# Kernel optimization log

Measured on AMD Instinct MI355X. Metric: run time of the kernel, lower is better.

Reference implementation:

```python
import jax, jax.numpy as jnp
import numpy as np

B = 256      # batch
C = 512      # num_classes (independent heads)
F = 768      # BERT pooler_output dim (hard-coded in module)
D = 512      # dense_layer_size


def setup_inputs() -> dict:
    key = jax.random.key(0)
    ks = jax.random.split(key, 7)
    s1 = 1.0 / np.sqrt(F)
    s2 = 1.0 / np.sqrt(D)
    return {
        "x":  jax.random.normal(ks[0], (B, F), dtype=jnp.float32),
        "W1": jax.random.normal(ks[1], (C, F, D), dtype=jnp.float32) * s1,
        "b1": jax.random.normal(ks[2], (C, D), dtype=jnp.float32) * s1,
        "W2": jax.random.normal(ks[3], (C, D, D), dtype=jnp.float32) * s2,
        "b2": jax.random.normal(ks[4], (C, D), dtype=jnp.float32) * s2,
        "W3": jax.random.normal(ks[5], (C, D, 2), dtype=jnp.float32) * s2,
        "b3": jax.random.normal(ks[6], (C, 2), dtype=jnp.float32) * s2,
    }


def reference(x, W1, b1, W2, b2, W3, b3):
    # Batched version of the per-class Python loop:
    # each head: Linear(F,D)-ReLU-(Dropout=identity in eval)-Linear(D,D)-ReLU-Linear(D,2)
    h = jax.nn.relu(jnp.einsum('bf,cfd->bcd', x, W1) + b1[None])        # [B, C, D]
    h = jax.nn.relu(jnp.einsum('bcd,cde->bce', h, W2) + b2[None])        # [B, C, D]
    out = jnp.einsum('bcd,cde->bce', h, W3) + b3[None]                   # [B, C, 2]
    return out
```

## Files before the change

### kernel.cpp

```cpp
#include <hip/hip_runtime.h>
#include <stdint.h>

typedef float f32x4 __attribute__((ext_vector_type(4)));
typedef float f32x2 __attribute__((ext_vector_type(2)));
typedef short bf16x8 __attribute__((ext_vector_type(8)));

__device__ __forceinline__ uint32_t bf16_rne(float f) {
  uint32_t x = __float_as_uint(f);
  return (x + 0x7FFFu + ((x >> 16) & 1u)) >> 16;
}

__device__ __forceinline__ void load_lds_16B(void* lds_dst, const void* gsrc) {
  __builtin_amdgcn_global_load_lds(
      (const __attribute__((address_space(1))) unsigned int*)gsrc,
      (__attribute__((address_space(3))) unsigned int*)lds_dst, 16, 0, 0);
}

__global__ void cast_x_kernel(const float* __restrict__ x,
                              uint32_t* __restrict__ xb, int n2) {
  int i = blockIdx.x * 256 + threadIdx.x;
  if (i >= n2) return;
  f32x2 v = *(const f32x2*)(x + 2 * i);
  xb[i] = bf16_rne(v[0]) | (bf16_rne(v[1]) << 16);
}

template <int K>
__global__ __launch_bounds__(512, 2) void gemm_relu(
    const uint16_t* __restrict__ Abase, long long aClassStride,
    const float* __restrict__ Wbase, const float* __restrict__ biasBase,
    uint16_t* __restrict__ Hout) {
  constexpr int NT = K / 64;
  __shared__ uint8_t smem[2 * 49152 + 512];

  const int tid = threadIdx.x;
  const int bid = blockIdx.x;
  const int logical = ((bid & 7) << 8) | (bid >> 3);
  const int c = logical >> 2;
  const int n0 = (logical & 3) * 128;

  const uint16_t* Ab = Abase + (size_t)c * (size_t)aClassStride;
  const float* Wc = Wbase + (size_t)c * K * 512 + n0;
  const float* bcp = biasBase + (size_t)c * 512 + n0;
  uint16_t* Oc = Hout + (size_t)c * (256 * 512) + n0;

  const int l = tid & 63, w = tid >> 6;
  const int lr = l & 15, lg = l >> 4;
  const int wm = w >> 1, wn = w & 1;

  const int aoff_row = (wm * 64 + lr) * 128;
  const int boff_row = 32768 + (wn * 64 + lr) * 128;
  const int kx0 = (lg * 16) ^ ((lr & 7) << 4);

  const int bcg = tid & 31;
  const int brp = tid >> 5;

  f32x4 acc[4][4];
#pragma unroll
  for (int i = 0; i < 4; i++)
#pragma unroll
    for (int j = 0; j < 4; j++) acc[i][j] = {0.f, 0.f, 0.f, 0.f};

  auto stageA = [&](int ts, int buf) {
    uint8_t* base = smem + buf * 49152;
    const uint16_t* As = Ab + ts * 64;
#pragma unroll
    for (int i = 0; i < 4; i++) {
      int idx = tid + i * 512;
      int m = idx >> 3, cc = idx & 7;
      int ccs = cc ^ (m & 7);
      load_lds_16B(base + ((w * 64 + i * 512) << 4),
                   As + (size_t)m * K + ccs * 8);
    }
  };
  auto loadB = [&](int ts, f32x4* br) {
    const float* Ws = Wc + (size_t)(ts * 64) * 512;
    br[0] = *(const f32x4*)(Ws + (size_t)(2 * brp) * 512 + 4 * bcg);
    br[1] = *(const f32x4*)(Ws + (size_t)(2 * brp + 1) * 512 + 4 * bcg);
    br[2] = *(const f32x4*)(Ws + (size_t)(2 * brp + 32) * 512 + 4 * bcg);
    br[3] = *(const f32x4*)(Ws + (size_t)(2 * brp + 33) * 512 + 4 * bcg);
  };
  auto writeB = [&](const f32x4* br, int buf) {
    uint8_t* base = smem + buf * 49152 + 32768;
#pragma unroll
    for (int u = 0; u < 2; u++) {
      int rp = brp + u * 16;
#pragma unroll
      for (int j = 0; j < 4; j++) {
        int n = 4 * bcg + j;
        uint32_t p = bf16_rne(br[2 * u][j]) | (bf16_rne(br[2 * u + 1][j]) << 16);
        *(uint32_t*)(base + n * 128 + ((4 * rp) ^ ((n & 7) << 4))) = p;
      }
    }
  };
  auto comp = [&](int buf) {
    const uint8_t* s = smem + buf * 49152;
#pragma unroll
    for (int kk = 0; kk < 2; ++kk) {
      const int kx = kx0 ^ (kk << 6);
      bf16x8 a[4], b[4];
#pragma unroll
      for (int mf = 0; mf < 4; mf++)
        a[mf] = *(const bf16x8*)(s + aoff_row + mf * 2048 + kx);
#pragma unroll
      for (int nf = 0; nf < 4; nf++)
        b[nf] = *(const bf16x8*)(s + boff_row + nf * 2048 + kx);
#pragma unroll
      for (int mf = 0; mf < 4; mf++)
#pragma unroll
        for (int nf = 0; nf < 4; nf++)
          acc[mf][nf] = __builtin_amdgcn_mfma_f32_16x16x32_bf16(
              a[mf], b[nf], acc[mf][nf], 0, 0, 0);
    }
  };

  f32x4 brA[4], brB[4];
  stageA(0, 0);
  loadB(0, brA);
  if (tid < 128) ((float*)(smem + 98304))[tid] = bcp[tid];
  writeB(brA, 0);
  __syncthreads();
  stageA(1, 1);
  loadB(1, brB);

#pragma unroll 1
  for (int t = 0; t < NT; t += 2) {
    comp(0);
    writeB(brB, 1);
    __syncthreads();
    if (t + 2 < NT) { stageA(t + 2, 0); loadB(t + 2, brA); }
    comp(1);
    if (t + 2 < NT) {
      writeB(brA, 0);
      __syncthreads();
      if (t + 3 < NT) { stageA(t + 3, 1); loadB(t + 3, brB); }
    }
  }

  const float* bs = (const float*)(smem + 98304);
#pragma unroll
  for (int mf = 0; mf < 4; mf++) {
#pragma unroll
    for (int nf = 0; nf < 4; nf++) {
      const int col = wn * 64 + nf * 16 + lr;
      const float bv = bs[col];
#pragma unroll
      for (int r = 0; r < 4; r++) {
        const int m = wm * 64 + mf * 16 + lg * 4 + r;
        float v = acc[mf][nf][r] + bv;
        v = fmaxf(v, 0.0f);
        Oc[(size_t)m * 512 + col] = (uint16_t)bf16_rne(v);
      }
    }
  }
}

__global__ __launch_bounds__(256) void head_kernel(
    const uint16_t* __restrict__ h2, const float* __restrict__ W3,
    const float* __restrict__ b3, float* __restrict__ out) {
  __shared__ float w3s[1024];
  __shared__ float b3s[2];
  const int c = blockIdx.x, t = threadIdx.x;
#pragma unroll
  for (int i = 0; i < 4; i++) w3s[t + i * 256] = W3[(size_t)c * 1024 + t + i * 256];
  if (t < 2) b3s[t] = b3[c * 2 + t];
  __syncthreads();
  const uint16_t* row = h2 + (size_t)c * 131072 + (size_t)t * 512;
  float a0 = b3s[0], a1 = b3s[1];
  for (int d = 0; d < 512; d += 8) {
    bf16x8 v = *(const bf16x8*)(row + d);
#pragma unroll
    for (int j = 0; j < 8; j++) {
      float f = __uint_as_float(((uint32_t)(uint16_t)v[j]) << 16);
      a0 += f * w3s[(d + j) * 2];
      a1 += f * w3s[(d + j) * 2 + 1];
    }
  }
  size_t o = ((size_t)t * 512 + c) * 2;
  out[o] = a0;
  out[o + 1] = a1;
}

extern "C" void kernel_launch(void* const* d_in, const int* in_sizes, int n_in,
                              void* d_out, int out_size, void* d_ws,
                              size_t ws_size, hipStream_t stream) {
  const float* x = (const float*)d_in[0];
  const float* W1 = (const float*)d_in[1];
  const float* b1 = (const float*)d_in[2];
  const float* W2 = (const float*)d_in[3];
  const float* b2 = (const float*)d_in[4];
  const float* W3 = (const float*)d_in[5];
  const float* b3 = (const float*)d_in[6];
  float* out = (float*)d_out;

  uint8_t* ws = (uint8_t*)d_ws;
  const size_t xb_off = 0;
  const size_t h1_off = 393216;
  const size_t h2_off = h1_off + 134217728;
  const size_t need = h2_off + 134217728;
  if (ws_size < need) return;

  uint32_t* xb = (uint32_t*)(ws + xb_off);
  uint16_t* h1 = (uint16_t*)(ws + h1_off);
  uint16_t* h2 = (uint16_t*)(ws + h2_off);

  cast_x_kernel<<<dim3(384), dim3(256), 0, stream>>>(x, xb, 98304);
  gemm_relu<768><<<dim3(2048), dim3(512), 0, stream>>>(
      (const uint16_t*)xb, 0LL, W1, b1, h1);
  gemm_relu<512><<<dim3(2048), dim3(512), 0, stream>>>(
      h1, 131072LL, W2, b2, h2);
  head_kernel<<<dim3(512), dim3(256), 0, stream>>>(h2, W3, b3, out);
}
```

Baseline: 456.3 us.

## Fuse final head into second GEMM epilogue and retile GEMMs to 256x64

Changes GEMM tiling from 256x128 per block to 256x64 (8 N-tiles per class, 4096 blocks), raising launch bounds occupancy to 4 blocks per CU and shrinking LDS. The B-load path is rewritten to per-lane scalar loads packed into 16-byte LDS writes. The second GEMM no longer writes h2; instead its epilogue applies bias+ReLU, dots with W3, shuffle-reduces across lanes and writes per-N-tile partial sums, reduced by a small kernel with b3. This removes the 128MB h2 write and re-read at the cost of a partial buffer and extra reduce launch.

After: 408.7 us. 10.4% less time.

```diff
diff --git a/kernel.cpp b/kernel.cpp
--- a/kernel.cpp
+++ b/kernel.cpp
@@ -4,6 +4,7 @@
 typedef float f32x4 __attribute__((ext_vector_type(4)));
 typedef float f32x2 __attribute__((ext_vector_type(2)));
 typedef short bf16x8 __attribute__((ext_vector_type(8)));
+typedef uint32_t u32x4 __attribute__((ext_vector_type(4)));
 
 __device__ __forceinline__ uint32_t bf16_rne(float f) {
   uint32_t x = __float_as_uint(f);
@@ -24,44 +25,36 @@
   xb[i] = bf16_rne(v[0]) | (bf16_rne(v[1]) << 16);
 }
 
-template <int K>
-__global__ __launch_bounds__(512, 2) void gemm_relu(
+template <int K, int MODE>
+__global__ __launch_bounds__(512, 4) void gemm_fused(
     const uint16_t* __restrict__ Abase, long long aClassStride,
     const float* __restrict__ Wbase, const float* __restrict__ biasBase,
-    uint16_t* __restrict__ Hout) {
+    uint16_t* __restrict__ Hout, const float* __restrict__ W3base,
+    float* __restrict__ part) {
   constexpr int NT = K / 64;
-  __shared__ uint8_t smem[2 * 49152 + 512];
+  __shared__ uint8_t smem[81920];
 
   const int tid = threadIdx.x;
   const int bid = blockIdx.x;
-  const int logical = ((bid & 7) << 8) | (bid >> 3);
-  const int c = logical >> 2;
-  const int n0 = (logical & 3) * 128;
+  const int logical = ((bid & 7) << 9) | (bid >> 3);
+  const int c = logical >> 3;
+  const int nt = logical & 7;
+  const int n0 = nt * 64;
 
   const uint16_t* Ab = Abase + (size_t)c * (size_t)aClassStride;
-  const float* Wc = Wbase + (size_t)c * K * 512 + n0;
-  const float* bcp = biasBase + (size_t)c * 512 + n0;
-  uint16_t* Oc = Hout + (size_t)c * (256 * 512) + n0;
+  const float* Wc = Wbase + (size_t)c * (K * 512) + n0;
 
   const int l = tid & 63, w = tid >> 6;
   const int lr = l & 15, lg = l >> 4;
-  const int wm = w >> 1, wn = w & 1;
-
-  const int aoff_row = (wm * 64 + lr) * 128;
-  const int boff_row = 32768 + (wn * 64 + lr) * 128;
-  const int kx0 = (lg * 16) ^ ((lr & 7) << 4);
-
-  const int bcg = tid & 31;
-  const int brp = tid >> 5;
-
-  f32x4 acc[4][4];
-#pragma unroll
-  for (int i = 0; i < 4; i++)
+
+  f32x4 acc[2][4];
+#pragma unroll
+  for (int i = 0; i < 2; i++)
 #pragma unroll
     for (int j = 0; j < 4; j++) acc[i][j] = {0.f, 0.f, 0.f, 0.f};
 
   auto stageA = [&](int ts, int buf) {
-    uint8_t* base = smem + buf * 49152;
+    uint8_t* base = smem + buf * 40960;
     const uint16_t* As = Ab + ts * 64;
 #pragma unroll
     for (int i = 0; i < 4; i++) {
@@ -72,40 +65,32 @@
                    As + (size_t)m * K + ccs * 8);
     }
   };
-  auto loadB = [&](int ts, f32x4* br) {
-    const float* Ws = Wc + (size_t)(ts * 64) * 512;
-    br[0] = *(const f32x4*)(Ws + (size_t)(2 * brp) * 512 + 4 * bcg);
-    br[1] = *(const f32x4*)(Ws + (size_t)(2 * brp + 1) * 512 + 4 * bcg);
-    br[2] = *(const f32x4*)(Ws + (size_t)(2 * brp + 32) * 512 + 4 * bcg);
-    br[3] = *(const f32x4*)(Ws + (size_t)(2 * brp + 33) * 512 + 4 * bcg);
-  };
-  auto writeB = [&](const f32x4* br, int buf) {
-    uint8_t* base = smem + buf * 49152 + 32768;
-#pragma unroll
-    for (int u = 0; u < 2; u++) {
-      int rp = brp + u * 16;
-#pragma unroll
-      for (int j = 0; j < 4; j++) {
-        int n = 4 * bcg + j;
-        uint32_t p = bf16_rne(br[2 * u][j]) | (bf16_rne(br[2 * u + 1][j]) << 16);
-        *(uint32_t*)(base + n * 128 + ((4 * rp) ^ ((n & 7) << 4))) = p;
-      }
-    }
+  auto loadB = [&](int ts, float* g) {
+    const float* Ws = Wc + (size_t)(ts * 64 + w * 8) * 512 + l;
+#pragma unroll
+    for (int r = 0; r < 8; r++) g[r] = Ws[(size_t)r * 512];
+  };
+  auto writeB = [&](const float* g, int buf) {
+    u32x4 p;
+#pragma unroll
+    for (int j = 0; j < 4; j++)
+      p[j] = bf16_rne(g[2 * j]) | (bf16_rne(g[2 * j + 1]) << 16);
+    *(u32x4*)(smem + buf * 40960 + 32768 + l * 128 + ((w ^ (l & 7)) << 4)) = p;
   };
   auto comp = [&](int buf) {
-    const uint8_t* s = smem + buf * 49152;
+    const uint8_t* s = smem + buf * 40960;
 #pragma unroll
     for (int kk = 0; kk < 2; ++kk) {
-      const int kx = kx0 ^ (kk << 6);
-      bf16x8 a[4], b[4];
-#pragma unroll
-      for (int mf = 0; mf < 4; mf++)
-        a[mf] = *(const bf16x8*)(s + aoff_row + mf * 2048 + kx);
+      const int kx = ((lg * 16) ^ ((lr & 7) << 4)) ^ (kk << 6);
+      bf16x8 a[2], b[4];
+#pragma unroll
+      for (int mf = 0; mf < 2; mf++)
+        a[mf] = *(const bf16x8*)(s + (w * 32 + mf * 16 + lr) * 128 + kx);
 #pragma unroll
       for (int nf = 0; nf < 4; nf++)
-        b[nf] = *(const bf16x8*)(s + boff_row + nf * 2048 + kx);
-#pragma unroll
-      for (int mf = 0; mf < 4; mf++)
+        b[nf] = *(const bf16x8*)(s + 32768 + (nf * 16 + lr) * 128 + kx);
+#pragma unroll
+      for (int mf = 0; mf < 2; mf++)
 #pragma unroll
         for (int nf = 0; nf < 4; nf++)
           acc[mf][nf] = __builtin_amdgcn_mfma_f32_16x16x32_bf16(
@@ -113,71 +98,90 @@
     }
   };
 
-  f32x4 brA[4], brB[4];
+  float g0[8], g1[8];
   stageA(0, 0);
-  loadB(0, brA);
-  if (tid < 128) ((float*)(smem + 98304))[tid] = bcp[tid];
-  writeB(brA, 0);
+  loadB(0, g0);
+  writeB(g0, 0);
   __syncthreads();
   stageA(1, 1);
-  loadB(1, brB);
+  loadB(1, g1);
 
 #pragma unroll 1
   for (int t = 0; t < NT; t += 2) {
     comp(0);
-    writeB(brB, 1);
+    writeB(g1, 1);
     __syncthreads();
-    if (t + 2 < NT) { stageA(t + 2, 0); loadB(t + 2, brA); }
+    if (t + 2 < NT) { stageA(t + 2, 0); loadB(t + 2, g0); }
     comp(1);
     if (t + 2 < NT) {
-      writeB(brA, 0);
+      writeB(g0, 0);
       __syncthreads();
-      if (t + 3 < NT) { stageA(t + 3, 1); loadB(t + 3, brB); }
+      if (t + 3 < NT) { stageA(t + 3, 1); loadB(t + 3, g1); }
     }
   }
 
-  const float* bs = (const float*)(smem + 98304);
-#pragma unroll
-  for (int mf = 0; mf < 4; mf++) {
+  float bv[4];
+#pragma unroll
+  for (int nf = 0; nf < 4; nf++)
+    bv[nf] = biasBase[c * 512 + n0 + nf * 16 + lr];
+
+  if constexpr (MODE == 0) {
+    uint16_t* Oc = Hout + (size_t)c * 131072 + n0;
+#pragma unroll
+    for (int mf = 0; mf < 2; mf++)
+#pragma unroll
+      for (int nf = 0; nf < 4; nf++)
+#pragma unroll
+        for (int r = 0; r < 4; r++) {
+          int m = w * 32 + mf * 16 + lg * 4 + r;
+          float v = fmaxf(acc[mf][nf][r] + bv[nf], 0.f);
+          Oc[(size_t)m * 512 + nf * 16 + lr] = (uint16_t)bf16_rne(v);
+        }
+  } else {
+    float w30[4], w31[4];
 #pragma unroll
     for (int nf = 0; nf < 4; nf++) {
-      const int col = wn * 64 + nf * 16 + lr;
-      const float bv = bs[col];
+      f32x2 t = *(const f32x2*)(W3base +
+                                ((size_t)c * 512 + n0 + nf * 16 + lr) * 2);
+      w30[nf] = t[0];
+      w31[nf] = t[1];
+    }
+#pragma unroll
+    for (int mf = 0; mf < 2; mf++)
 #pragma unroll
       for (int r = 0; r < 4; r++) {
-        const int m = wm * 64 + mf * 16 + lg * 4 + r;
-        float v = acc[mf][nf][r] + bv;
-        v = fmaxf(v, 0.0f);
-        Oc[(size_t)m * 512 + col] = (uint16_t)bf16_rne(v);
+        float s0 = 0.f, s1 = 0.f;
+#pragma unroll
+        for (int nf = 0; nf < 4; nf++) {
+          float v = fmaxf(acc[mf][nf][r] + bv[nf], 0.f);
+          s0 += v * w30[nf];
+          s1 += v * w31[nf];
+        }
+#pragma unroll
+        for (int d = 1; d < 16; d <<= 1) {
+          s0 += __shfl_xor(s0, d);
+          s1 += __shfl_xor(s1, d);
+        }
+        if (lr == 0) {
+          int m = w * 32 + mf * 16 + lg * 4 + r;
+          *(f32x2*)(part + (((size_t)c * 256 + m) * 8 + nt) * 2) =
+              f32x2{s0, s1};
+        }
       }
-    }
   }
 }
 
-__global__ __launch_bounds__(256) void head_kernel(
-    const uint16_t* __restrict__ h2, const float* __restrict__ W3,
-    const float* __restrict__ b3, float* __restrict__ out) {
-  __shared__ float w3s[1024];
-  __shared__ float b3s[2];
-  const int c = blockIdx.x, t = threadIdx.x;
-#pragma unroll
-  for (int i = 0; i < 4; i++) w3s[t + i * 256] = W3[(size_t)c * 1024 + t + i * 256];
-  if (t < 2) b3s[t] = b3[c * 2 + t];
-  __syncthreads();
-  const uint16_t* row = h2 + (size_t)c * 131072 + (size_t)t * 512;
-  float a0 = b3s[0], a1 = b3s[1];
-  for (int d = 0; d < 512; d += 8) {
-    bf16x8 v = *(const bf16x8*)(row + d);
-#pragma unroll
-    for (int j = 0; j < 8; j++) {
-      float f = __uint_as_float(((uint32_t)(uint16_t)v[j]) << 16);
-      a0 += f * w3s[(d + j) * 2];
-      a1 += f * w3s[(d + j) * 2 + 1];
-    }
-  }
-  size_t o = ((size_t)t * 512 + c) * 2;
-  out[o] = a0;
-  out[o + 1] = a1;
+__global__ __launch_bounds__(512) void reduce_out(
+    const float* __restrict__ part, const float* __restrict__ b3,
+    float* __restrict__ out) {
+  const int b = blockIdx.x, c = threadIdx.x;
+  const f32x4* p = (const f32x4*)(part + ((size_t)c * 256 + b) * 16);
+  f32x4 v0 = p[0], v1 = p[1], v2 = p[2], v3 = p[3];
+  float s0 = b3[c * 2] + v0[0] + v0[2] + v1[0] + v1[2] + v2[0] + v2[2] +
+             v3[0] + v3[2];
+  float s1 = b3[c * 2 + 1] + v0[1] + v0[3] + v1[1] + v1[3] + v2[1] + v2[3] +
+             v3[1] + v3[3];
+  *(f32x2*)(out + ((size_t)b * 512 + c) * 2) = f32x2{s0, s1};
 }
 
 extern "C" void kernel_launch(void* const* d_in, const int* in_sizes, int n_in,
@@ -195,18 +199,18 @@
   uint8_t* ws = (uint8_t*)d_ws;
   const size_t xb_off = 0;
   const size_t h1_off = 393216;
-  const size_t h2_off = h1_off + 134217728;
-  const size_t need = h2_off + 134217728;
+  const size_t part_off = h1_off + 134217728;
+  const size_t need = part_off + 8388608;
   if (ws_size < need) return;
 
   uint32_t* xb = (uint32_t*)(ws + xb_off);
   uint16_t* h1 = (uint16_t*)(ws + h1_off);
-  uint16_t* h2 = (uint16_t*)(ws + h2_off);
+  float* part = (float*)(ws + part_off);
 
   cast_x_kernel<<<dim3(384), dim3(256), 0, stream>>>(x, xb, 98304);
-  gemm_relu<768><<<dim3(2048), dim3(512), 0, stream>>>(
-      (const uint16_t*)xb, 0LL, W1, b1, h1);
-  gemm_relu<512><<<dim3(2048), dim3(512), 0, stream>>>(
-      h1, 131072LL, W2, b2, h2);
-  head_kernel<<<dim3(512), dim3(256), 0, stream>>>(h2, W3, b3, out);
-}
+  gemm_fused<768, 0><<<dim3(4096), dim3(512), 0, stream>>>(
+      (const uint16_t*)xb, 0LL, W1, b1, h1, nullptr, nullptr);
+  gemm_fused<512, 1><<<dim3(4096), dim3(512), 0, stream>>>(
+      h1, 131072LL, W2, b2, nullptr, W3, part);
+  reduce_out<<<dim3(256), dim3(512), 0, stream>>>(part, b3, out);
+}
```
